# Performance work log

Hardware: AMD Instinct MI355X
Metric: run time of the kernel (lower is better)

The kernel has to match this reference:

```python
import jax, jax.numpy as jnp
import numpy as np
from jax import lax

N = 100000   # input points
M = 100000   # output points
CIN = 64
COUT = 64
K = 3        # cubic kernel size
G = 50       # grid side (points live at voxel centers of a G^3 grid)
SHIFT = 1    # coordinate shift so border queries (coord -1) stay non-negative
B = 64       # per-axis encode base, > G + K; key fits easily in int32


def _encode(c):
    # c: [..., 3] int32 xyz voxel coords -> unique int32 key
    c = c + SHIFT
    return (c[..., 2] * B + c[..., 1]) * B + c[..., 0]


def setup_inputs() -> dict:
    rng = np.random.RandomState(0)
    total = G ** 3

    def decode(idx):
        x = idx % G
        y = (idx // G) % G
        z = idx // (G * G)
        # +0.5 moves points to voxel centers (as in the layer's docstring example)
        return np.stack([x, y, z], axis=1).astype(np.float32) + 0.5

    inp_positions = jnp.asarray(decode(rng.permutation(total)[:N]))
    out_positions = jnp.asarray(decode(rng.permutation(total)[:M]))

    key = jax.random.key(0)
    k1, k2 = jax.random.split(key, 2)
    inp_features = jax.random.normal(k1, (N, CIN), jnp.float32)
    kernel = jax.random.normal(k2, (K, K, K, CIN, COUT), jnp.float32) * 0.05
    bias = jnp.zeros((COUT,), jnp.float32)
    voxel_size = jnp.ones((), jnp.float32)
    return {
        "inp_features": inp_features,
        "inp_positions": inp_positions,
        "out_positions": out_positions,
        "voxel_size": voxel_size,
        "kernel": kernel,
        "bias": bias,
    }


def reference(inp_features, inp_positions, out_positions, voxel_size, kernel, bias):
    # SparseConv on a regular grid: odd cubic kernel -> offset = 0, Linf radius
    # K*voxel*0.51 selects exactly the K^3 voxel neighborhood. Nearest-neighbor
    # interpolation with identity mapping maps relative offset d in [-r, r]^3
    # to filter tap index d + r on each axis (x = width = last spatial dim).
    inp_coord = jnp.floor(inp_positions / voxel_size).astype(jnp.int32)  # [N,3]
    out_coord = jnp.floor(out_positions / voxel_size).astype(jnp.int32)  # [M,3]

    # sorted-key hash table over input voxels
    keys = _encode(inp_coord)                    # [N]
    order = jnp.argsort(keys)
    skeys = keys[order]
    feats = inp_features[order]                  # [N, Cin]

    r = K // 2
    K3 = K ** 3
    ks = jnp.arange(K3)
    # flat kernel order is (z, y, x) to match kernel.reshape(K3, Cin, Cout)
    d_xyz = jnp.stack([ks % K - r, (ks // K) % K - r, ks // (K * K) - r],
                      axis=1).astype(jnp.int32)  # [K3, 3]
    Kmat = kernel.reshape(K3, CIN, COUT)

    n_inp = skeys.shape[0]

    def step(acc, xs):
        d, W = xs                                 # d: [3], W: [Cin, Cout]
        qk = _encode(out_coord + d)               # [M]
        p = jnp.searchsorted(skeys, qk)
        pc = jnp.clip(p, 0, n_inp - 1)
        found = (skeys[pc] == qk)[:, None]        # [M, 1]
        g = jnp.where(found, feats[pc], 0.0)      # [M, Cin]
        return acc + g @ W, None

    out0 = jnp.zeros((out_coord.shape[0], COUT), inp_features.dtype)
    out, _ = lax.scan(step, out0, (d_xyz, Kmat))
    return out + bias
```

## Files before the change

kernel.cpp:

```cpp
#include <hip/hip_runtime.h>
#include <math.h>

#define GY 54
#define NROWS (54*54*64)

#define HX 10
#define HY 6
#define NH 360
#define NBX 7
#define NBY 13
#define NBRICK (7*13*13)
#define SLAB 148

#define LDK 72

typedef __bf16  bf16x8 __attribute__((ext_vector_type(8)));
typedef float  f32x16 __attribute__((ext_vector_type(16)));

__global__ void prep_kernel(const float* __restrict__ ipos, int n,
                            const float* __restrict__ opos, int m,
                            const float* __restrict__ vsp,
                            const float* __restrict__ W,
                            int* __restrict__ imap, int* __restrict__ omap,
                            __bf16* __restrict__ Wt) {
    int i = blockIdx.x * 256 + threadIdx.x;
    float vs = vsp[0];
    if (i < n) {
        int x = (int)floorf(ipos[3*i+0] / vs) + 1;
        int y = (int)floorf(ipos[3*i+1] / vs) + 1;
        int z = (int)floorf(ipos[3*i+2] / vs) + 1;
        imap[(z * GY + y) * 64 + x] = i;
    } else if (i < n + m) {
        int j = i - n;
        int x = (int)floorf(opos[3*j+0] / vs) + 1;
        int y = (int)floorf(opos[3*j+1] / vs) + 1;
        int z = (int)floorf(opos[3*j+2] / vs) + 1;
        omap[(z * GY + y) * 64 + x] = j;
    } else if (i < n + m + 27*64*64) {
        int k  = i - n - m;
        int t  = k >> 12;
        int r  = k & 4095;
        int ci = r >> 6;
        int co = r & 63;
        Wt[(t << 12) + (co << 6) + ci] = (__bf16)W[k];
    }
}

__global__ __launch_bounds__(256, 2) void conv_kernel(
    const float* __restrict__ feats,
    const __bf16* __restrict__ Wt,
    const float* __restrict__ bias,
    const int*   __restrict__ imap,
    const int*   __restrict__ omap,
    float*       __restrict__ out)
{
    __shared__ __align__(16) __bf16 halo[NH * LDK];
    __shared__ __align__(16) __bf16 Bld[2][64 * LDK];
    __shared__ int obuf[128];

    const int tid = threadIdx.x;

    int q = (blockIdx.x & 7) * SLAB + (blockIdx.x >> 3);
    if (q >= NBRICK) return;
    const int bx = q % NBX;
    int rem = q / NBX;
    const int by = rem % NBY;
    const int bz = rem / NBY;

    const int wr0 = tid >> 3;
    const int wr1 = 32 + wr0;
    const int wc  = tid & 7;

    float4 wreg0 = *(const float4*)(Wt + wr0 * 64 + wc * 8);
    float4 wreg1 = *(const float4*)(Wt + wr1 * 64 + wc * 8);
    *(float4*)(&Bld[0][wr0 * LDK + wc * 8]) = wreg0;
    *(float4*)(&Bld[0][wr1 * LDK + wc * 8]) = wreg1;
    wreg0 = *(const float4*)(Wt + 4096 + wr0 * 64 + wc * 8);
    wreg1 = *(const float4*)(Wt + 4096 + wr1 * 64 + wc * 8);

    #pragma unroll
    for (int it = 0; it < 12; ++it) {
        int task = it * 256 + tid;
        if (task < NH * 8) {
            int r = task >> 3, c = task & 7;
            int xs = r % HX;
            int t2 = r / HX;
            int ys = t2 % HY;
            int zs = t2 / HY;
            int key = ((bz*4 + zs) * GY + (by*4 + ys)) * 64 + (bx*8 + xs);
            int idx = imap[key];
            bf16x8 v;
            if (idx >= 0) {
                const float4* s = (const float4*)(feats + (size_t)idx * 64 + c * 8);
                float4 f0 = s[0], f1 = s[1];
                v[0]=(__bf16)f0.x; v[1]=(__bf16)f0.y; v[2]=(__bf16)f0.z; v[3]=(__bf16)f0.w;
                v[4]=(__bf16)f1.x; v[5]=(__bf16)f1.y; v[6]=(__bf16)f1.z; v[7]=(__bf16)f1.w;
            } else {
                #pragma unroll
                for (int j = 0; j < 8; ++j) v[j] = (__bf16)0.f;
            }
            *(bf16x8*)(halo + r * LDK + c * 8) = v;
        }
    }
    if (tid < 128) {
        int x = tid & 7, y = (tid >> 3) & 3, z = tid >> 5;
        int key = ((bz*4 + z + 1) * GY + (by*4 + y + 1)) * 64 + (bx*8 + x + 1);
        obuf[tid] = omap[key];
    }

    const int wave  = tid >> 6;
    const int lane  = tid & 63;
    const int lrow  = lane & 31;
    const int halfk = lane >> 5;
    const int xv = lrow & 7, yv = (lrow >> 3) & 3;
    const int r0 = (wave + 1) * (HX*HY) + (yv + 1) * HX + (xv + 1);
    const __bf16* Abase = halo + r0 * LDK + halfk * 8;
    const int Bb0 = lrow * LDK + halfk * 8;
    const int Bb1 = (32 + lrow) * LDK + halfk * 8;

    f32x16 acc0, acc1;
    #pragma unroll
    for (int i = 0; i < 16; ++i) { acc0[i] = 0.f; acc1[i] = 0.f; }

    __syncthreads();

    #pragma unroll 1
    for (int t = 0; t < 27; ++t) {
        if (t < 26) {
            __bf16* nb = &Bld[(t + 1) & 1][0];
            *(float4*)(nb + wr0 * LDK + wc * 8) = wreg0;
            *(float4*)(nb + wr1 * LDK + wc * 8) = wreg1;
        }
        if (t < 25) {
            const __bf16* wp = Wt + ((size_t)(t + 2) << 12);
            wreg0 = *(const float4*)(wp + wr0 * 64 + wc * 8);
            wreg1 = *(const float4*)(wp + wr1 * 64 + wc * 8);
        }

        const int dx = t % 3 - 1;
        const int dy = (t / 3) % 3 - 1;
        const int dz = t / 9 - 1;
        const __bf16* Ab = Abase + (dz * (HX*HY) + dy * HX + dx) * LDK;
        const __bf16* Bbuf = &Bld[t & 1][0];

        #pragma unroll
        for (int kc = 0; kc < 4; ++kc) {
            bf16x8 a  = *(const bf16x8*)(Ab + kc * 16);
            bf16x8 b0 = *(const bf16x8*)(Bbuf + Bb0 + kc * 16);
            bf16x8 b1 = *(const bf16x8*)(Bbuf + Bb1 + kc * 16);
            acc0 = __builtin_amdgcn_mfma_f32_32x32x16_bf16(a, b0, acc0, 0, 0, 0);
            acc1 = __builtin_amdgcn_mfma_f32_32x32x16_bf16(a, b1, acc1, 0, 0, 0);
        }
        __syncthreads();
    }

    const int col0 = lrow, col1 = 32 + lrow;
    const float bv0 = bias[col0], bv1 = bias[col1];
    #pragma unroll
    for (int r = 0; r < 16; ++r) {
        int row = (r & 3) + 8 * (r >> 2) + 4 * halfk;
        int orow = obuf[wave * 32 + row];
        if (orow >= 0) {
            out[(size_t)orow * 64 + col0] = acc0[r] + bv0;
            out[(size_t)orow * 64 + col1] = acc1[r] + bv1;
        }
    }
}

extern "C" void kernel_launch(void* const* d_in, const int* in_sizes, int n_in,
                              void* d_out, int out_size, void* d_ws, size_t ws_size,
                              hipStream_t stream) {
    const float* feats = (const float*)d_in[0];
    const float* ipos  = (const float*)d_in[1];
    const float* opos  = (const float*)d_in[2];
    const float* vsp   = (const float*)d_in[3];
    const float* W     = (const float*)d_in[4];
    const float* bias  = (const float*)d_in[5];

    int N = in_sizes[0] / 64;
    int M = out_size / 64;

    int*    imap = (int*)d_ws;
    int*    omap = imap + NROWS;
    __bf16* Wt   = (__bf16*)(omap + NROWS);

    hipMemsetAsync(imap, 0xFF, (size_t)2 * NROWS * sizeof(int), stream);
    int total = N + M + 27*64*64;
    prep_kernel<<<(total + 255) / 256, 256, 0, stream>>>(ipos, N, opos, M, vsp, W,
                                                         imap, omap, Wt);
    conv_kernel<<<8 * SLAB, 256, 0, stream>>>(feats, Wt, bias, imap, omap, (float*)d_out);
}
```

Measured before the change: 148.9 us.

## Double brick depth per block and replace map memset with key validation

Each block now handles an 8x4x8 brick instead of 8x4x4. Each wave computes two 32-row M tiles that share the B fragments, so the halo overhead and per-block weight streaming are amortized over twice the outputs. The memset of the dense index maps is removed. Stale map entries are instead filtered by checking the stored per-point key arrays, which trades a large clear for extra dependent gathers. Occupancy drops to one block per CU because of the larger LDS halo and the doubled accumulators.

After: 169.7 us. +14.0%, slower.

```diff
diff --git a/kernel.cpp b/kernel.cpp
--- a/kernel.cpp
+++ b/kernel.cpp
@@ -2,15 +2,18 @@
 #include <math.h>
 
 #define GY 54
-#define NROWS (54*54*64)
+#define ZD 58
+#define NROWS (ZD*GY*64)
 
 #define HX 10
 #define HY 6
-#define NH 360
+#define HXY 60
+#define NH 600
 #define NBX 7
 #define NBY 13
-#define NBRICK (7*13*13)
-#define SLAB 148
+#define NBZ 7
+#define NBRICK (NBX*NBY*NBZ)
+#define SLAB 80
 
 #define LDK 72
 
@@ -21,7 +24,8 @@
                             const float* __restrict__ opos, int m,
                             const float* __restrict__ vsp,
                             const float* __restrict__ W,
-                            int* __restrict__ imap, int* __restrict__ omap,
+                            int* __restrict__ imap, int* __restrict__ ikey,
+                            int* __restrict__ omap, int* __restrict__ okey,
                             __bf16* __restrict__ Wt) {
     int i = blockIdx.x * 256 + threadIdx.x;
     float vs = vsp[0];
@@ -29,13 +33,17 @@
         int x = (int)floorf(ipos[3*i+0] / vs) + 1;
         int y = (int)floorf(ipos[3*i+1] / vs) + 1;
         int z = (int)floorf(ipos[3*i+2] / vs) + 1;
-        imap[(z * GY + y) * 64 + x] = i;
+        int key = (z * GY + y) * 64 + x;
+        ikey[i] = key;
+        imap[key] = i;
     } else if (i < n + m) {
         int j = i - n;
         int x = (int)floorf(opos[3*j+0] / vs) + 1;
         int y = (int)floorf(opos[3*j+1] / vs) + 1;
         int z = (int)floorf(opos[3*j+2] / vs) + 1;
-        omap[(z * GY + y) * 64 + x] = j;
+        int key = (z * GY + y) * 64 + x;
+        okey[j] = key;
+        omap[key] = j;
     } else if (i < n + m + 27*64*64) {
         int k  = i - n - m;
         int t  = k >> 12;
@@ -46,17 +54,21 @@
     }
 }
 
-__global__ __launch_bounds__(256, 2) void conv_kernel(
+__global__ __launch_bounds__(256, 1) void conv_kernel(
     const float* __restrict__ feats,
     const __bf16* __restrict__ Wt,
     const float* __restrict__ bias,
     const int*   __restrict__ imap,
+    const int*   __restrict__ ikey,
     const int*   __restrict__ omap,
-    float*       __restrict__ out)
+    const int*   __restrict__ okey,
+    float*       __restrict__ out,
+    int N, int M)
 {
     __shared__ __align__(16) __bf16 halo[NH * LDK];
     __shared__ __align__(16) __bf16 Bld[2][64 * LDK];
-    __shared__ int obuf[128];
+    __shared__ int ridx[NH];
+    __shared__ int obuf[256];
 
     const int tid = threadIdx.x;
 
@@ -79,16 +91,34 @@
     wreg1 = *(const float4*)(Wt + 4096 + wr1 * 64 + wc * 8);
 
     #pragma unroll
-    for (int it = 0; it < 12; ++it) {
-        int task = it * 256 + tid;
-        if (task < NH * 8) {
-            int r = task >> 3, c = task & 7;
+    for (int it = 0; it < 3; ++it) {
+        int r = it * 256 + tid;
+        if (r < NH) {
             int xs = r % HX;
             int t2 = r / HX;
             int ys = t2 % HY;
             int zs = t2 / HY;
-            int key = ((bz*4 + zs) * GY + (by*4 + ys)) * 64 + (bx*8 + xs);
+            int key = ((bz*8 + zs) * GY + (by*4 + ys)) * 64 + (bx*8 + xs);
             int idx = imap[key];
+            int c = min(max(idx, 0), N - 1);
+            ridx[r] = (idx >= 0 && idx < N && ikey[c] == key) ? idx : -1;
+        }
+    }
+    {
+        int x = tid & 7, y = (tid >> 3) & 3, z = tid >> 5;
+        int key = ((bz*8 + z + 1) * GY + (by*4 + y + 1)) * 64 + (bx*8 + x + 1);
+        int o = omap[key];
+        int c = min(max(o, 0), M - 1);
+        obuf[tid] = (o >= 0 && o < M && okey[c] == key) ? o : -1;
+    }
+    __syncthreads();
+
+    #pragma unroll
+    for (int it = 0; it < 19; ++it) {
+        int task = it * 256 + tid;
+        if (task < NH * 8) {
+            int r = task >> 3, c = task & 7;
+            int idx = ridx[r];
             bf16x8 v;
             if (idx >= 0) {
                 const float4* s = (const float4*)(feats + (size_t)idx * 64 + c * 8);
@@ -102,25 +132,20 @@
             *(bf16x8*)(halo + r * LDK + c * 8) = v;
         }
     }
-    if (tid < 128) {
-        int x = tid & 7, y = (tid >> 3) & 3, z = tid >> 5;
-        int key = ((bz*4 + z + 1) * GY + (by*4 + y + 1)) * 64 + (bx*8 + x + 1);
-        obuf[tid] = omap[key];
-    }
 
     const int wave  = tid >> 6;
     const int lane  = tid & 63;
     const int lrow  = lane & 31;
     const int halfk = lane >> 5;
-    const int xv = lrow & 7, yv = (lrow >> 3) & 3;
-    const int r0 = (wave + 1) * (HX*HY) + (yv + 1) * HX + (xv + 1);
-    const __bf16* Abase = halo + r0 * LDK + halfk * 8;
+    const int xv = lrow & 7, yv = lrow >> 3;
+    const __bf16* A0base = halo + ((2*wave + 1) * HXY + (yv + 1) * HX + (xv + 1)) * LDK
+                                + halfk * 8;
     const int Bb0 = lrow * LDK + halfk * 8;
-    const int Bb1 = (32 + lrow) * LDK + halfk * 8;
-
-    f32x16 acc0, acc1;
-    #pragma unroll
-    for (int i = 0; i < 16; ++i) { acc0[i] = 0.f; acc1[i] = 0.f; }
+    const int Bb1 = Bb0 + 32 * LDK;
+
+    f32x16 acc00, acc01, acc10, acc11;
+    #pragma unroll
+    for (int i = 0; i < 16; ++i) { acc00[i]=0.f; acc01[i]=0.f; acc10[i]=0.f; acc11[i]=0.f; }
 
     __syncthreads();
 
@@ -140,16 +165,20 @@
         const int dx = t % 3 - 1;
         const int dy = (t / 3) % 3 - 1;
         const int dz = t / 9 - 1;
-        const __bf16* Ab = Abase + (dz * (HX*HY) + dy * HX + dx) * LDK;
+        const __bf16* Ab0 = A0base + (dz * HXY + dy * HX + dx) * LDK;
+        const __bf16* Ab1 = Ab0 + HXY * LDK;
         const __bf16* Bbuf = &Bld[t & 1][0];
 
         #pragma unroll
         for (int kc = 0; kc < 4; ++kc) {
-            bf16x8 a  = *(const bf16x8*)(Ab + kc * 16);
+            bf16x8 a0 = *(const bf16x8*)(Ab0 + kc * 16);
+            bf16x8 a1 = *(const bf16x8*)(Ab1 + kc * 16);
             bf16x8 b0 = *(const bf16x8*)(Bbuf + Bb0 + kc * 16);
             bf16x8 b1 = *(const bf16x8*)(Bbuf + Bb1 + kc * 16);
-            acc0 = __builtin_amdgcn_mfma_f32_32x32x16_bf16(a, b0, acc0, 0, 0, 0);
-            acc1 = __builtin_amdgcn_mfma_f32_32x32x16_bf16(a, b1, acc1, 0, 0, 0);
+            acc00 = __builtin_amdgcn_mfma_f32_32x32x16_bf16(a0, b0, acc00, 0, 0, 0);
+            acc01 = __builtin_amdgcn_mfma_f32_32x32x16_bf16(a0, b1, acc01, 0, 0, 0);
+            acc10 = __builtin_amdgcn_mfma_f32_32x32x16_bf16(a1, b0, acc10, 0, 0, 0);
+            acc11 = __builtin_amdgcn_mfma_f32_32x32x16_bf16(a1, b1, acc11, 0, 0, 0);
         }
         __syncthreads();
     }
@@ -158,11 +187,17 @@
     const float bv0 = bias[col0], bv1 = bias[col1];
     #pragma unroll
     for (int r = 0; r < 16; ++r) {
-        int row = (r & 3) + 8 * (r >> 2) + 4 * halfk;
-        int orow = obuf[wave * 32 + row];
-        if (orow >= 0) {
-            out[(size_t)orow * 64 + col0] = acc0[r] + bv0;
-            out[(size_t)orow * 64 + col1] = acc1[r] + bv1;
+        int mrow = (r & 3) + 8 * (r >> 2) + 4 * halfk;
+        int v0 = (2*wave) * 32 + mrow;
+        int o0 = obuf[v0];
+        int o1 = obuf[v0 + 32];
+        if (o0 >= 0) {
+            out[(size_t)o0 * 64 + col0] = acc00[r] + bv0;
+            out[(size_t)o0 * 64 + col1] = acc01[r] + bv1;
+        }
+        if (o1 >= 0) {
+            out[(size_t)o1 * 64 + col0] = acc10[r] + bv0;
+            out[(size_t)o1 * 64 + col1] = acc11[r] + bv1;
         }
     }
 }
@@ -182,11 +217,13 @@
 
     int*    imap = (int*)d_ws;
     int*    omap = imap + NROWS;
-    __bf16* Wt   = (__bf16*)(omap + NROWS);
-
-    hipMemsetAsync(imap, 0xFF, (size_t)2 * NROWS * sizeof(int), stream);
+    int*    ikey = omap + NROWS;
+    int*    okey = ikey + N;
+    __bf16* Wt   = (__bf16*)(okey + M);
+
     int total = N + M + 27*64*64;
     prep_kernel<<<(total + 255) / 256, 256, 0, stream>>>(ipos, N, opos, M, vsp, W,
-                                                         imap, omap, Wt);
-    conv_kernel<<<8 * SLAB, 256, 0, stream>>>(feats, Wt, bias, imap, omap, (float*)d_out);
+                                                         imap, ikey, omap, okey, Wt);
+    conv_kernel<<<8 * SLAB, 256, 0, stream>>>(feats, Wt, bias, imap, ikey, omap, okey,
+                                              (float*)d_out, N, M);
 }
```
